# Optimization experiments

Hardware: AMD Instinct MI355X
Metric: run time of the kernel (lower is better)

## Reference

```python
import jax, jax.numpy as jnp
import numpy as np

B, D, H, W = 16, 512, 32, 32
M = 2000
TEMP_UPDATE = 0.1
TEMP_GATHER = 0.1


def l2norm(x, axis, eps=1e-12):
    # matches F.normalize: x / max(||x||_2, eps)
    n = jnp.linalg.norm(x, axis=axis, keepdims=True)
    return x / jnp.maximum(n, eps)


def setup_inputs() -> dict:
    key = jax.random.key(0)
    k1, k2 = jax.random.split(key)
    query = jax.random.normal(k1, (B, D, H, W), dtype=jnp.float32)
    # memory bank initialized as F.normalize(randn) * 0.1, as in __init__
    keys = l2norm(jax.random.normal(k2, (M, D), dtype=jnp.float32), axis=1) * 0.1
    return {"query": query, "keys": keys}


def reference(query, keys):
    b, d, h, w = query.shape
    m = keys.shape[0]
    # normalize along channels, move to [B,H,W,D], flatten to [N,D]
    q = jnp.transpose(l2norm(query, axis=1), (0, 2, 3, 1))
    qf = q.reshape(b * h * w, d)  # [N, D]

    # --- get_score (same score reused by gather_loss / read / update) ---
    score = l2norm(qf, axis=1) @ l2norm(keys, axis=1).T  # [N, M] cosine sims
    tg = min(max(TEMP_GATHER, 1e-8), 1.0)
    tu = min(max(TEMP_UPDATE, 1e-8), 1.0)
    score_query = jax.nn.softmax(score / tg, axis=0)   # softmax over queries
    score_memory = jax.nn.softmax(score / tu, axis=1)  # softmax over memory slots

    # --- gather_loss (train) ---
    _, top2 = jax.lax.top_k(score_memory, 2)  # [N, 2]
    pos = jax.lax.stop_gradient(keys[top2[:, 0]])
    neg = jax.lax.stop_gradient(keys[top2[:, 1]])
    compactness_loss = jnp.mean((qf - pos) ** 2)
    # TripletMarginLoss(margin=1.0), torch pairwise_distance eps=1e-6
    dp = jnp.sqrt(jnp.sum((qf - pos + 1e-6) ** 2, axis=-1))
    dn = jnp.sqrt(jnp.sum((qf - neg + 1e-6) ** 2, axis=-1))
    separateness_loss = jnp.mean(jnp.maximum(dp - dn + 1.0, 0.0))

    # --- read ---
    concat_memory = jax.lax.stop_gradient(score_memory) @ keys  # [N, D]
    updated_query = jnp.concatenate([qf, concat_memory], axis=1)
    updated_query = jnp.transpose(updated_query.reshape(b, h, w, 2 * d), (0, 3, 1, 2))

    # --- update (vectorized get_update_query: per-slot gather + weighted sum) ---
    g = top2[:, 0]  # top-1 gathering index per query, [N]
    col_max = jnp.max(score_query, axis=0)  # [M]
    w_raw = jnp.take_along_axis(score_query, g[:, None], axis=1)[:, 0] / (col_max[g] + 1e-8)
    denom = jax.ops.segment_sum(w_raw, g, num_segments=m) + 1e-8  # [M]
    weights = w_raw / denom[g]
    query_update = jax.ops.segment_sum(weights[:, None] * qf, g, num_segments=m)  # [M, D]
    updated_memory = jax.lax.stop_gradient(l2norm(query_update + keys, axis=1))

    return (updated_query, updated_memory, score_query, score_memory,
            separateness_loss, compactness_loss)
```

## Files before the change

### kernel.cpp

```cpp
#include <hip/hip_runtime.h>
#include <math.h>

#define NQ 16384
#define DD 512
#define MM 2000
#define MPAD 2048
#define KPAD 2048

#define UQ_OFF   0
#define UM_OFF   16777216
#define SQ_OFF   17801216
#define SM_OFF   50569216
#define SEP_OFF  83337216
#define COMP_OFF 83337217

typedef unsigned short u16;
typedef __attribute__((ext_vector_type(8))) short bhalf8;
typedef __attribute__((ext_vector_type(4))) float f32x4;

__device__ float    g_qf[NQ * DD];
__device__ float    g_keyshat[MM * DD];
__device__ int      g_top1[NQ];
__device__ int      g_top2[NQ];
__device__ unsigned g_colmax[MM];
__device__ float    g_colsum[MM];
__device__ float    g_rowsum[NQ];
__device__ float    g_wraw[NQ];
__device__ float    g_denom[MM];
__device__ float    g_bins[128];
__device__ int      g_cnt[MM];
__device__ int      g_cursor[MM];
__device__ int      g_base[MM];
__device__ int      g_rows[NQ];
__device__ float    g_wvals[NQ];

__device__ __attribute__((aligned(16))) u16 g_qh[NQ * DD];
__device__ __attribute__((aligned(16))) u16 g_ql[NQ * DD];
__device__ __attribute__((aligned(16))) u16 g_kh[MPAD * DD];
__device__ __attribute__((aligned(16))) u16 g_kl[MPAD * DD];
__device__ __attribute__((aligned(16))) u16 g_kth[DD * KPAD];
__device__ __attribute__((aligned(16))) u16 g_ktl[DD * KPAD];
__device__ __attribute__((aligned(16))) u16 g_smh[(size_t)NQ * KPAD];
__device__ __attribute__((aligned(16))) u16 g_sml[(size_t)NQ * KPAD];

__device__ inline u16 f32_to_bf16(float x) {
    unsigned u = __float_as_uint(x);
    return (u16)((u + 0x7fffu + ((u >> 16) & 1u)) >> 16);
}
__device__ inline float bf16f(u16 h) { return __uint_as_float((unsigned)h << 16); }

__device__ __forceinline__ void gl_lds16(const void* g, void* l) {
    __builtin_amdgcn_global_load_lds(
        (const __attribute__((address_space(1))) void*)g,
        (__attribute__((address_space(3))) void*)l, 16, 0, 0);
}

__global__ __launch_bounds__(256) void init_kernel() {
    int i = blockIdx.x * 256 + threadIdx.x;
    if (i < MM) { g_colsum[i] = 0.f; g_denom[i] = 0.f; g_colmax[i] = 0u;
                  g_cnt[i] = 0; g_cursor[i] = 0; }
    if (i < 128) g_bins[i] = 0.f;
    if (i < NQ) g_rowsum[i] = 0.f;
}

__global__ __launch_bounds__(256) void keys_norm_kernel(const float* __restrict__ keys) {
    int m = blockIdx.x, t = threadIdx.x;
    float v0 = keys[m * DD + t], v1 = keys[m * DD + t + 256];
    __shared__ float red[256];
    red[t] = v0 * v0 + v1 * v1;
    __syncthreads();
    for (int s = 128; s > 0; s >>= 1) { if (t < s) red[t] += red[t + s]; __syncthreads(); }
    float inv = 1.f / fmaxf(sqrtf(red[0]), 1e-12f);
    float n0 = v0 * inv, n1 = v1 * inv;
    g_keyshat[m * DD + t]       = n0;
    g_keyshat[m * DD + t + 256] = n1;
    u16 h0 = f32_to_bf16(n0), h1 = f32_to_bf16(n1);
    g_kh[(size_t)m * DD + t]       = h0;
    g_kl[(size_t)m * DD + t]       = f32_to_bf16(n0 - bf16f(h0));
    g_kh[(size_t)m * DD + t + 256] = h1;
    g_kl[(size_t)m * DD + t + 256] = f32_to_bf16(n1 - bf16f(h1));
}

__global__ __launch_bounds__(256) void ktrans_kernel(const float* __restrict__ keys) {
    __shared__ float tile[32][33];
    int tx = threadIdx.x & 31, ty = threadIdx.x >> 5;
    int c0 = blockIdx.x * 32;
    int m0 = blockIdx.y * 32;
    for (int i = ty; i < 32; i += 8) {
        int m = m0 + i;
        tile[i][tx] = (m < MM) ? keys[(size_t)m * DD + c0 + tx] : 0.f;
    }
    __syncthreads();
    for (int i = ty; i < 32; i += 8) {
        int c = c0 + i;
        float v = tile[tx][i];
        u16 h = f32_to_bf16(v);
        g_kth[(size_t)c * KPAD + m0 + tx] = h;
        g_ktl[(size_t)c * KPAD + m0 + tx] = f32_to_bf16(v - bf16f(h));
    }
}

__global__ __launch_bounds__(256) void qnorm_kernel(const float* __restrict__ q, float* __restrict__ out) {
    int bh = blockIdx.x; int b = bh >> 5, h = bh & 31;
    int t = threadIdx.x; int w = t & 31, dl = t >> 5;
    const float* qb = q + (size_t)b * DD * 1024 + h * 32;

    float ss = 0.f;
    for (int d = dl; d < DD; d += 8) { float v = qb[d * 1024 + w]; ss = fmaf(v, v, ss); }
    __shared__ float red[8][32];
    __shared__ float sinv[32];
    red[dl][w] = ss;
    __syncthreads();
    if (dl == 0) {
        float tot = 0.f;
        #pragma unroll
        for (int j = 0; j < 8; ++j) tot += red[j][w];
        sinv[w] = 1.f / fmaxf(sqrtf(tot), 1e-12f);
    }
    __syncthreads();

    __shared__ float tile[32][33];
    int dcol = t & 31, wl = t >> 5;
    for (int d0 = 0; d0 < DD; d0 += 32) {
        for (int dd = dl; dd < 32; dd += 8) {
            float v = qb[(d0 + dd) * 1024 + w] * sinv[w];
            tile[dd][w] = v;
            out[UQ_OFF + (size_t)((b << 10) + d0 + dd) * 1024 + (h << 5) + w] = v;
        }
        __syncthreads();
        for (int wr = wl; wr < 32; wr += 8) {
            float v = tile[dcol][wr];
            size_t idx = ((size_t)b * 1024 + h * 32 + wr) * DD + d0 + dcol;
            g_qf[idx] = v;
            u16 hh = f32_to_bf16(v);
            g_qh[idx] = hh;
            g_ql[idx] = f32_to_bf16(v - bf16f(hh));
        }
        __syncthreads();
    }
}

__device__ inline void mfma_block(const u16 (*Ah)[64], const u16 (*Al)[64],
                                  const u16 (*Bh)[64], const u16 (*Bl)[64],
                                  int wr, int wc, int l15, int hi, f32x4 acc[4][4]) {
    for (int sub = 0; sub < 2; ++sub) {
        bhalf8 a_h[4], a_l[4], b_h[4], b_l[4];
        #pragma unroll
        for (int i = 0; i < 4; ++i) {
            int r = wr + i * 16 + l15;
            int ps = (((sub << 2) | hi) ^ (r & 7)) << 3;
            a_h[i] = *(const bhalf8*)&Ah[r][ps];
            a_l[i] = *(const bhalf8*)&Al[r][ps];
        }
        #pragma unroll
        for (int j = 0; j < 4; ++j) {
            int c = wc + j * 16 + l15;
            int ps = (((sub << 2) | hi) ^ (c & 7)) << 3;
            b_h[j] = *(const bhalf8*)&Bh[c][ps];
            b_l[j] = *(const bhalf8*)&Bl[c][ps];
        }
        #pragma unroll
        for (int i = 0; i < 4; ++i)
            #pragma unroll
            for (int j = 0; j < 4; ++j) {
                acc[i][j] = __builtin_amdgcn_mfma_f32_16x16x32_bf16(a_h[i], b_h[j], acc[i][j], 0, 0, 0);
                acc[i][j] = __builtin_amdgcn_mfma_f32_16x16x32_bf16(a_h[i], b_l[j], acc[i][j], 0, 0, 0);
                acc[i][j] = __builtin_amdgcn_mfma_f32_16x16x32_bf16(a_l[i], b_h[j], acc[i][j], 0, 0, 0);
            }
    }
}

__global__ __launch_bounds__(256, 2) void gemm1_mfma(float* __restrict__ out) {
    __shared__ __attribute__((aligned(16))) u16 Ah[128][64];
    __shared__ __attribute__((aligned(16))) u16 Al[128][64];
    __shared__ __attribute__((aligned(16))) u16 Bh[128][64];
    __shared__ __attribute__((aligned(16))) u16 Bl[128][64];
    int t = threadIdx.x;
    int lane = t & 63, wv = t >> 6;
    int wr = (wv >> 1) << 6, wc = (wv & 1) << 6;
    int l15 = lane & 15, hi = lane >> 4;
    int row0 = blockIdx.x * 128;
    int col0 = blockIdx.y * 128;

    f32x4 acc[4][4] = {};
    int lr = lane >> 3, sslot = lane & 7;
    int xs = sslot ^ lr;

    for (int k0 = 0; k0 < DD; k0 += 64) {
        #pragma unroll
        for (int p = 0; p < 4; ++p) {
            int r = wv * 8 + lr + p * 32;
            size_t ga = (size_t)(row0 + r) * DD + k0 + xs * 8;
            size_t gb = (size_t)(col0 + r) * DD + k0 + xs * 8;
            gl_lds16(g_qh + ga, &Ah[p * 32 + wv * 8][0]);
            gl_lds16(g_ql + ga, &Al[p * 32 + wv * 8][0]);
            gl_lds16(g_kh + gb, &Bh[p * 32 + wv * 8][0]);
            gl_lds16(g_kl + gb, &Bl[p * 32 + wv * 8][0]);
        }
        __syncthreads();
        mfma_block(Ah, Al, Bh, Bl, wr, wc, l15, hi, acc);
        __syncthreads();
    }

    float rowp[4][4];
    #pragma unroll
    for (int i = 0; i < 4; ++i)
        #pragma unroll
        for (int q = 0; q < 4; ++q) rowp[i][q] = 0.f;

    #pragma unroll
    for (int j = 0; j < 4; ++j) {
        int c = col0 + wc + j * 16 + l15;
        bool valid = (c < MM);
        float cs = 0.f, cm = 0.f;
        #pragma unroll
        for (int i = 0; i < 4; ++i) {
            int rbase = row0 + wr + i * 16 + hi * 4;
            #pragma unroll
            for (int q = 0; q < 4; ++q) {
                float e = __expf((acc[i][j][q] - 1.0f) * 10.0f);
                if (valid) out[SQ_OFF + (size_t)(rbase + q) * MM + c] = e;
                float ev = valid ? e : 0.f;
                rowp[i][q] += ev;
                cs += ev;
                cm = fmaxf(cm, ev);
            }
        }
        cs += __shfl_xor(cs, 16); cs += __shfl_xor(cs, 32);
        cm = fmaxf(cm, __shfl_xor(cm, 16)); cm = fmaxf(cm, __shfl_xor(cm, 32));
        if (hi == 0 && valid) {
            atomicAdd(&g_colsum[c], cs);
            atomicMax(&g_colmax[c], __float_as_uint(cm));
        }
    }
    #pragma unroll
    for (int i = 0; i < 4; ++i)
        #pragma unroll
        for (int q = 0; q < 4; ++q) {
            float v = rowp[i][q];
            v += __shfl_xor(v, 1); v += __shfl_xor(v, 2);
            v += __shfl_xor(v, 4); v += __shfl_xor(v, 8);
            if (l15 == 0) atomicAdd(&g_rowsum[row0 + wr + i * 16 + hi * 4 + q], v);
        }
}

__global__ __launch_bounds__(256) void rowpass_kernel(float* __restrict__ out) {
    int n = blockIdx.x, t = threadIdx.x;
    __shared__ float rv[256], rv2[256];
    __shared__ int   ri[256], ri2[256];
    float inv_rs = 1.f / g_rowsum[n];
    float* raw = out + SQ_OFF + (size_t)n * MM;
    float* sm  = out + SM_OFF + (size_t)n * MM;
    float v1 = -1.f, v2 = -1.f; int i1 = 0x7fffffff, i2 = 0x7fffffff;
    #pragma unroll
    for (int i = 0; i < 8; ++i) {
        int idx = i * 256 + t;
        if (idx < MM) {
            float e = raw[idx];
            if (e > v1)      { v2 = v1; i2 = i1; v1 = e; i1 = idx; }
            else if (e > v2) { v2 = e; i2 = idx; }
            float smv = e * inv_rs;
            sm[idx] = smv;
            u16 hh = f32_to_bf16(smv);
            g_smh[(size_t)n * KPAD + idx] = hh;
            g_sml[(size_t)n * KPAD + idx] = f32_to_bf16(smv - bf16f(hh));
            raw[idx] = e / g_colsum[idx];
        }
    }
    rv[t] = v1; ri[t] = i1; rv2[t] = v2; ri2[t] = i2;
    __syncthreads();
    for (int s = 128; s > 0; s >>= 1) {
        if (t < s) {
            float av1 = rv[t],  bv1 = rv[t + s];
            float av2 = rv2[t], bv2 = rv2[t + s];
            int   ai1 = ri[t],  bi1 = ri[t + s];
            int   ai2 = ri2[t], bi2 = ri2[t + s];
            bool afirst = (av1 > bv1) || (av1 == bv1 && ai1 < bi1);
            float nv1, nv2; int ni1, ni2;
            if (afirst) {
                nv1 = av1; ni1 = ai1;
                if ((av2 > bv1) || (av2 == bv1 && ai2 < bi1)) { nv2 = av2; ni2 = ai2; }
                else                                          { nv2 = bv1; ni2 = bi1; }
            } else {
                nv1 = bv1; ni1 = bi1;
                if ((bv2 > av1) || (bv2 == av1 && bi2 < ai1)) { nv2 = bv2; ni2 = bi2; }
                else                                          { nv2 = av1; ni2 = ai1; }
            }
            rv[t] = nv1; ri[t] = ni1; rv2[t] = nv2; ri2[t] = ni2;
        }
        __syncthreads();
    }
    if (t == 0) { g_top1[n] = ri[0]; g_top2[n] = ri2[0]; }
}

__global__ __launch_bounds__(256) void rerank_loss_kernel(const float* __restrict__ keys) {
    int n = blockIdx.x * 4 + (threadIdx.x >> 6);
    int lane = threadIdx.x & 63;
    int i1 = g_top1[n], i2 = g_top2[n];
    const float* q  = g_qf      + (size_t)n  * DD;
    const float* k1 = g_keyshat + (size_t)i1 * DD;
    const float* k2 = g_keyshat + (size_t)i2 * DD;
    float s1 = 0.f, s2 = 0.f;
    #pragma unroll
    for (int kk = 0; kk < 8; ++kk) {
        int k = lane + kk * 64;
        float qv = q[k];
        s1 = fmaf(qv, k1[k], s1);
        s2 = fmaf(qv, k2[k], s2);
    }
    #pragma unroll
    for (int off = 1; off < 64; off <<= 1) {
        s1 += __shfl_xor(s1, off);
        s2 += __shfl_xor(s2, off);
    }
    bool sw = (s2 > s1) || (s2 == s1 && i2 < i1);
    int gi = sw ? i2 : i1, ni = sw ? i1 : i2;
    if (lane == 0 && sw) { g_top1[n] = i2; g_top2[n] = i1; }
    const float* kp = keys + (size_t)gi * DD;
    const float* kn = keys + (size_t)ni * DD;
    float comp = 0.f, dpp = 0.f, dnn = 0.f;
    #pragma unroll
    for (int kk = 0; kk < 8; ++kk) {
        int k = lane + kk * 64;
        float qv = q[k];
        float dq = qv - kp[k];
        comp = fmaf(dq, dq, comp);
        float a = dq + 1e-6f;
        dpp = fmaf(a, a, dpp);
        float b2 = qv - kn[k] + 1e-6f;
        dnn = fmaf(b2, b2, dnn);
    }
    #pragma unroll
    for (int off = 1; off < 64; off <<= 1) {
        comp += __shfl_xor(comp, off);
        dpp  += __shfl_xor(dpp,  off);
        dnn  += __shfl_xor(dnn,  off);
    }
    if (lane == 0) {
        float dp = sqrtf(dpp), dn = sqrtf(dnn);
        atomicAdd(&g_bins[n & 63], fmaxf(dp - dn + 1.0f, 0.0f));
        atomicAdd(&g_bins[64 + (n & 63)], comp);
    }
}

__global__ __launch_bounds__(256) void wraw_kernel(const float* __restrict__ out) {
    int n = blockIdx.x * 256 + threadIdx.x;
    int gi = g_top1[n];
    float sqv = out[SQ_OFF + (size_t)n * MM + gi];
    float cm = __uint_as_float(g_colmax[gi]) / g_colsum[gi];
    float w = sqv / (cm + 1e-8f);
    g_wraw[n] = w;
    atomicAdd(&g_denom[gi], w);
    atomicAdd(&g_cnt[gi], 1);
}

__global__ __launch_bounds__(256) void scan_kernel() {
    int t = threadIdx.x;
    __shared__ int chunk[256];
    __shared__ int off[256];
    int loc[8];
    int s = 0;
    #pragma unroll
    for (int i = 0; i < 8; ++i) {
        int idx = t * 8 + i;
        int c = (idx < MM) ? g_cnt[idx] : 0;
        loc[i] = s; s += c;
    }
    chunk[t] = s;
    __syncthreads();
    if (t == 0) {
        int acc = 0;
        for (int i = 0; i < 256; ++i) { off[i] = acc; acc += chunk[i]; }
    }
    __syncthreads();
    #pragma unroll
    for (int i = 0; i < 8; ++i) {
        int idx = t * 8 + i;
        if (idx < MM) g_base[idx] = off[t] + loc[i];
    }
}

__global__ __launch_bounds__(256) void scatter_kernel() {
    int n = blockIdx.x * 256 + threadIdx.x;
    int gi = g_top1[n];
    int pos = atomicAdd(&g_cursor[gi], 1);
    int dst = g_base[gi] + pos;
    g_rows[dst]  = n;
    g_wvals[dst] = g_wraw[n];
}

__global__ __launch_bounds__(256) void seg_update_kernel(const float* __restrict__ keys, float* __restrict__ out) {
    int m = blockIdx.x, t = threadIdx.x;
    int start = g_base[m], cnt = g_cnt[m];
    float invd = 1.f / (g_denom[m] + 1e-8f);
    float acc0 = 0.f, acc1 = 0.f;
    for (int i = 0; i < cnt; ++i) {
        int   row = g_rows[start + i];
        float wgt = g_wvals[start + i] * invd;
        acc0 = fmaf(wgt, g_qf[(size_t)row * DD + t],       acc0);
        acc1 = fmaf(wgt, g_qf[(size_t)row * DD + t + 256], acc1);
    }
    float v0 = acc0 + keys[m * DD + t];
    float v1 = acc1 + keys[m * DD + t + 256];
    __shared__ float red[256];
    red[t] = v0 * v0 + v1 * v1;
    __syncthreads();
    for (int s = 128; s > 0; s >>= 1) { if (t < s) red[t] += red[t + s]; __syncthreads(); }
    float inv = 1.f / fmaxf(sqrtf(red[0]), 1e-12f);
    out[UM_OFF + (size_t)m * DD + t]       = v0 * inv;
    out[UM_OFF + (size_t)m * DD + t + 256] = v1 * inv;
}

__global__ __launch_bounds__(256, 2) void gemm2_mfma(float* __restrict__ out) {
    __shared__ __attribute__((aligned(16))) u16 Ah[128][64];
    __shared__ __attribute__((aligned(16))) u16 Al[128][64];
    __shared__ __attribute__((aligned(16))) u16 Bh[128][64];
    __shared__ __attribute__((aligned(16))) u16 Bl[128][64];
    int t = threadIdx.x;
    int lane = t & 63, wv = t >> 6;
    int wr = (wv >> 1) << 6, wc = (wv & 1) << 6;
    int l15 = lane & 15, hi = lane >> 4;
    int row0 = blockIdx.x * 128;
    int col0 = blockIdx.y * 128;

    f32x4 acc[4][4] = {};
    int lr = lane >> 3, sslot = lane & 7;
    int xs = sslot ^ lr;

    for (int k0 = 0; k0 < KPAD; k0 += 64) {
        #pragma unroll
        for (int p = 0; p < 4; ++p) {
            int r = wv * 8 + lr + p * 32;
            size_t ga = (size_t)(row0 + r) * KPAD + k0 + xs * 8;
            size_t gb = (size_t)(col0 + r) * KPAD + k0 + xs * 8;
            gl_lds16(g_kth + ga, &Ah[p * 32 + wv * 8][0]);
            gl_lds16(g_ktl + ga, &Al[p * 32 + wv * 8][0]);
            gl_lds16(g_smh + gb, &Bh[p * 32 + wv * 8][0]);
            gl_lds16(g_sml + gb, &Bl[p * 32 + wv * 8][0]);
        }
        __syncthreads();
        mfma_block(Ah, Al, Bh, Bl, wr, wc, l15, hi, acc);
        __syncthreads();
    }
    int bq = col0 >> 10;
    #pragma unroll
    for (int i = 0; i < 4; ++i) {
        int chb = row0 + wr + i * 16 + hi * 4;
        #pragma unroll
        for (int j = 0; j < 4; ++j) {
            int n = col0 + wc + j * 16 + l15;
            size_t base = UQ_OFF + ((size_t)(bq * 1024 + 512 + chb)) * 1024 + (n & 1023);
            #pragma unroll
            for (int q = 0; q < 4; ++q)
                out[base + (size_t)q * 1024] = acc[i][j][q];
        }
    }
}

__global__ __launch_bounds__(64) void finalize_kernel(float* __restrict__ out) {
    if (threadIdx.x == 0) {
        float s = 0.f, c = 0.f;
        for (int i = 0; i < 64; ++i) { s += g_bins[i]; c += g_bins[64 + i]; }
        out[SEP_OFF]  = s / (float)NQ;
        out[COMP_OFF] = c / ((float)NQ * (float)DD);
    }
}

extern "C" void kernel_launch(void* const* d_in, const int* in_sizes, int n_in,
                              void* d_out, int out_size, void* d_ws, size_t ws_size,
                              hipStream_t stream) {
    const float* query = (const float*)d_in[0];
    const float* keys  = (const float*)d_in[1];
    float* out = (float*)d_out;

    init_kernel<<<dim3(64), dim3(256), 0, stream>>>();
    keys_norm_kernel<<<dim3(MM), dim3(256), 0, stream>>>(keys);
    ktrans_kernel<<<dim3(16, 63), dim3(256), 0, stream>>>(keys);
    qnorm_kernel<<<dim3(512), dim3(256), 0, stream>>>(query, out);
    gemm1_mfma<<<dim3(128, 16), dim3(256), 0, stream>>>(out);
    rowpass_kernel<<<dim3(NQ), dim3(256), 0, stream>>>(out);
    rerank_loss_kernel<<<dim3(NQ / 4), dim3(256), 0, stream>>>(keys);
    wraw_kernel<<<dim3(64), dim3(256), 0, stream>>>(out);
    scan_kernel<<<dim3(1), dim3(256), 0, stream>>>();
    scatter_kernel<<<dim3(64), dim3(256), 0, stream>>>();
    seg_update_kernel<<<dim3(MM), dim3(256), 0, stream>>>(keys, out);
    gemm2_mfma<<<dim3(4, 128), dim3(256), 0, stream>>>(out);
    finalize_kernel<<<dim3(1), dim3(64), 0, stream>>>(out);
}
```

Before: 971.9 us.

## Store unnormalized exp scores as split bf16, defer row normalization, double-buffer GEMMs

gemm1 now writes the exponentiated scores as hi/lo bf16 pairs into the GEMM2 operand buffers instead of fp32 to the output. The row pass reads these back with vector loads to produce both softmax outputs. gemm2 consumes the unnormalized scores and applies the per-row inverse sum in its epilogue. Both GEMMs switch to a K=32 double-buffered LDS pipeline that overlaps the next stage's loads with MFMA, and qnorm handles 64 pixels per block; together these cut fp32 round-trips and expose memory latency less, at the cost of a slight bf16-split rounding on score values.

```diff
diff --git a/kernel.cpp b/kernel.cpp
--- a/kernel.cpp
+++ b/kernel.cpp
@@ -25,6 +25,7 @@
 __device__ unsigned g_colmax[MM];
 __device__ float    g_colsum[MM];
 __device__ float    g_rowsum[NQ];
+__device__ float    g_invrs[NQ];
 __device__ float    g_wraw[NQ];
 __device__ float    g_denom[MM];
 __device__ float    g_bins[128];
@@ -101,36 +102,41 @@
 }
 
 __global__ __launch_bounds__(256) void qnorm_kernel(const float* __restrict__ q, float* __restrict__ out) {
-    int bh = blockIdx.x; int b = bh >> 5, h = bh & 31;
-    int t = threadIdx.x; int w = t & 31, dl = t >> 5;
-    const float* qb = q + (size_t)b * DD * 1024 + h * 32;
+    int blk = blockIdx.x;
+    int b = blk >> 4, hp = blk & 15;
+    int r0 = hp * 64;
+    int t = threadIdx.x;
+    int px = t & 63, ds = t >> 6;
+    const float* qb = q + (size_t)b * DD * 1024 + r0;
 
     float ss = 0.f;
-    for (int d = dl; d < DD; d += 8) { float v = qb[d * 1024 + w]; ss = fmaf(v, v, ss); }
-    __shared__ float red[8][32];
-    __shared__ float sinv[32];
-    red[dl][w] = ss;
-    __syncthreads();
-    if (dl == 0) {
-        float tot = 0.f;
-        #pragma unroll
-        for (int j = 0; j < 8; ++j) tot += red[j][w];
-        sinv[w] = 1.f / fmaxf(sqrtf(tot), 1e-12f);
-    }
-    __syncthreads();
-
-    __shared__ float tile[32][33];
-    int dcol = t & 31, wl = t >> 5;
+    for (int d = ds; d < DD; d += 4) { float v = qb[(size_t)d * 1024 + px]; ss = fmaf(v, v, ss); }
+    __shared__ float red[4][64];
+    __shared__ float sinv[64];
+    red[ds][px] = ss;
+    __syncthreads();
+    if (ds == 0) {
+        float tot = red[0][px] + red[1][px] + red[2][px] + red[3][px];
+        sinv[px] = 1.f / fmaxf(sqrtf(tot), 1e-12f);
+    }
+    __syncthreads();
+
+    __shared__ float tile[32][65];
+    int dcol = t & 31, pl = t >> 5;
     for (int d0 = 0; d0 < DD; d0 += 32) {
-        for (int dd = dl; dd < 32; dd += 8) {
-            float v = qb[(d0 + dd) * 1024 + w] * sinv[w];
-            tile[dd][w] = v;
-            out[UQ_OFF + (size_t)((b << 10) + d0 + dd) * 1024 + (h << 5) + w] = v;
+        #pragma unroll
+        for (int k = 0; k < 8; ++k) {
+            int dd = ds * 8 + k;
+            float v = qb[(size_t)(d0 + dd) * 1024 + px] * sinv[px];
+            tile[dd][px] = v;
+            out[UQ_OFF + (size_t)((b << 10) + d0 + dd) * 1024 + r0 + px] = v;
         }
         __syncthreads();
-        for (int wr = wl; wr < 32; wr += 8) {
-            float v = tile[dcol][wr];
-            size_t idx = ((size_t)b * 1024 + h * 32 + wr) * DD + d0 + dcol;
+        #pragma unroll
+        for (int pr = 0; pr < 8; ++pr) {
+            int px2 = pr * 8 + pl;
+            float v = tile[dcol][px2];
+            size_t idx = ((size_t)b * 1024 + r0 + px2) * DD + d0 + dcol;
             g_qf[idx] = v;
             u16 hh = f32_to_bf16(v);
             g_qh[idx] = hh;
@@ -140,65 +146,72 @@
     }
 }
 
-__device__ inline void mfma_block(const u16 (*Ah)[64], const u16 (*Al)[64],
-                                  const u16 (*Bh)[64], const u16 (*Bl)[64],
-                                  int wr, int wc, int l15, int hi, f32x4 acc[4][4]) {
-    for (int sub = 0; sub < 2; ++sub) {
-        bhalf8 a_h[4], a_l[4], b_h[4], b_l[4];
-        #pragma unroll
-        for (int i = 0; i < 4; ++i) {
-            int r = wr + i * 16 + l15;
-            int ps = (((sub << 2) | hi) ^ (r & 7)) << 3;
-            a_h[i] = *(const bhalf8*)&Ah[r][ps];
-            a_l[i] = *(const bhalf8*)&Al[r][ps];
-        }
+__device__ __forceinline__ void stage_pair(const u16* __restrict__ gh, const u16* __restrict__ gl,
+                                           u16 (*th)[32], u16 (*tl)[32],
+                                           size_t grow0, size_t ld, int kk, int wv, int lane) {
+    #pragma unroll
+    for (int p = 0; p < 2; ++p) {
+        int rbase = wv * 32 + p * 16;
+        int row = rbase + (lane >> 2);
+        int slot = (lane & 3) ^ ((row >> 1) & 3);
+        size_t off = (grow0 + row) * ld + (size_t)kk * 32 + slot * 8;
+        gl_lds16(gh + off, &th[rbase][0]);
+        gl_lds16(gl + off, &tl[rbase][0]);
+    }
+}
+
+__device__ __forceinline__ bhalf8 frag(const u16 (*tile)[32], int r, int hi) {
+    int ps = (hi ^ ((r >> 1) & 3)) << 3;
+    return *(const bhalf8*)&tile[r][ps];
+}
+
+__device__ __forceinline__ void mfma_phase(const u16 (*Ah)[32], const u16 (*Al)[32],
+                                           const u16 (*Bh)[32], const u16 (*Bl)[32],
+                                           int wr, int wc, int l15, int hi, f32x4 acc[4][4]) {
+    bhalf8 a_h[4], a_l[4], b_h[4], b_l[4];
+    #pragma unroll
+    for (int i = 0; i < 4; ++i) {
+        int r = wr + i * 16 + l15;
+        a_h[i] = frag(Ah, r, hi); a_l[i] = frag(Al, r, hi);
+    }
+    #pragma unroll
+    for (int j = 0; j < 4; ++j) {
+        int c = wc + j * 16 + l15;
+        b_h[j] = frag(Bh, c, hi); b_l[j] = frag(Bl, c, hi);
+    }
+    #pragma unroll
+    for (int i = 0; i < 4; ++i)
         #pragma unroll
         for (int j = 0; j < 4; ++j) {
-            int c = wc + j * 16 + l15;
-            int ps = (((sub << 2) | hi) ^ (c & 7)) << 3;
-            b_h[j] = *(const bhalf8*)&Bh[c][ps];
-            b_l[j] = *(const bhalf8*)&Bl[c][ps];
-        }
-        #pragma unroll
-        for (int i = 0; i < 4; ++i)
-            #pragma unroll
-            for (int j = 0; j < 4; ++j) {
-                acc[i][j] = __builtin_amdgcn_mfma_f32_16x16x32_bf16(a_h[i], b_h[j], acc[i][j], 0, 0, 0);
-                acc[i][j] = __builtin_amdgcn_mfma_f32_16x16x32_bf16(a_h[i], b_l[j], acc[i][j], 0, 0, 0);
-                acc[i][j] = __builtin_amdgcn_mfma_f32_16x16x32_bf16(a_l[i], b_h[j], acc[i][j], 0, 0, 0);
-            }
-    }
-}
-
-__global__ __launch_bounds__(256, 2) void gemm1_mfma(float* __restrict__ out) {
-    __shared__ __attribute__((aligned(16))) u16 Ah[128][64];
-    __shared__ __attribute__((aligned(16))) u16 Al[128][64];
-    __shared__ __attribute__((aligned(16))) u16 Bh[128][64];
-    __shared__ __attribute__((aligned(16))) u16 Bl[128][64];
-    int t = threadIdx.x;
-    int lane = t & 63, wv = t >> 6;
+            acc[i][j] = __builtin_amdgcn_mfma_f32_16x16x32_bf16(a_h[i], b_h[j], acc[i][j], 0, 0, 0);
+            acc[i][j] = __builtin_amdgcn_mfma_f32_16x16x32_bf16(a_h[i], b_l[j], acc[i][j], 0, 0, 0);
+            acc[i][j] = __builtin_amdgcn_mfma_f32_16x16x32_bf16(a_l[i], b_h[j], acc[i][j], 0, 0, 0);
+        }
+}
+
+__global__ __launch_bounds__(256, 2) void gemm1_mfma() {
+    __shared__ __attribute__((aligned(16))) u16 Ah[2][128][32];
+    __shared__ __attribute__((aligned(16))) u16 Al[2][128][32];
+    __shared__ __attribute__((aligned(16))) u16 Bh[2][128][32];
+    __shared__ __attribute__((aligned(16))) u16 Bl[2][128][32];
+    int t = threadIdx.x, lane = t & 63, wv = t >> 6;
     int wr = (wv >> 1) << 6, wc = (wv & 1) << 6;
     int l15 = lane & 15, hi = lane >> 4;
     int row0 = blockIdx.x * 128;
     int col0 = blockIdx.y * 128;
 
     f32x4 acc[4][4] = {};
-    int lr = lane >> 3, sslot = lane & 7;
-    int xs = sslot ^ lr;
-
-    for (int k0 = 0; k0 < DD; k0 += 64) {
-        #pragma unroll
-        for (int p = 0; p < 4; ++p) {
-            int r = wv * 8 + lr + p * 32;
-            size_t ga = (size_t)(row0 + r) * DD + k0 + xs * 8;
-            size_t gb = (size_t)(col0 + r) * DD + k0 + xs * 8;
-            gl_lds16(g_qh + ga, &Ah[p * 32 + wv * 8][0]);
-            gl_lds16(g_ql + ga, &Al[p * 32 + wv * 8][0]);
-            gl_lds16(g_kh + gb, &Bh[p * 32 + wv * 8][0]);
-            gl_lds16(g_kl + gb, &Bl[p * 32 + wv * 8][0]);
-        }
-        __syncthreads();
-        mfma_block(Ah, Al, Bh, Bl, wr, wc, l15, hi, acc);
+    stage_pair(g_qh, g_ql, Ah[0], Al[0], row0, DD, 0, wv, lane);
+    stage_pair(g_kh, g_kl, Bh[0], Bl[0], col0, DD, 0, wv, lane);
+    __syncthreads();
+    #pragma unroll 2
+    for (int kk = 0; kk < 16; ++kk) {
+        int cb = kk & 1, nb = cb ^ 1;
+        if (kk < 15) {
+            stage_pair(g_qh, g_ql, Ah[nb], Al[nb], row0, DD, kk + 1, wv, lane);
+            stage_pair(g_kh, g_kl, Bh[nb], Bl[nb], col0, DD, kk + 1, wv, lane);
+        }
+        mfma_phase(Ah[cb], Al[cb], Bh[cb], Bl[cb], wr, wc, l15, hi, acc);
         __syncthreads();
     }
 
@@ -219,8 +232,14 @@
             #pragma unroll
             for (int q = 0; q < 4; ++q) {
                 float e = __expf((acc[i][j][q] - 1.0f) * 10.0f);
-                if (valid) out[SQ_OFF + (size_t)(rbase + q) * MM + c] = e;
-                float ev = valid ? e : 0.f;
+                u16 eh = f32_to_bf16(e);
+                u16 el = f32_to_bf16(e - bf16f(eh));
+                float er = bf16f(eh) + bf16f(el);
+                if (valid) {
+                    g_smh[(size_t)(rbase + q) * KPAD + c] = eh;
+                    g_sml[(size_t)(rbase + q) * KPAD + c] = el;
+                }
+                float ev = valid ? er : 0.f;
                 rowp[i][q] += ev;
                 cs += ev;
                 cm = fmaxf(cm, ev);
@@ -246,25 +265,36 @@
 
 __global__ __launch_bounds__(256) void rowpass_kernel(float* __restrict__ out) {
     int n = blockIdx.x, t = threadIdx.x;
+    float inv_rs = 1.f / g_rowsum[n];
+    if (t == 0) g_invrs[n] = inv_rs;
     __shared__ float rv[256], rv2[256];
     __shared__ int   ri[256], ri2[256];
-    float inv_rs = 1.f / g_rowsum[n];
-    float* raw = out + SQ_OFF + (size_t)n * MM;
-    float* sm  = out + SM_OFF + (size_t)n * MM;
-    float v1 = -1.f, v2 = -1.f; int i1 = 0x7fffffff, i2 = 0x7fffffff;
-    #pragma unroll
-    for (int i = 0; i < 8; ++i) {
-        int idx = i * 256 + t;
-        if (idx < MM) {
-            float e = raw[idx];
-            if (e > v1)      { v2 = v1; i2 = i1; v1 = e; i1 = idx; }
-            else if (e > v2) { v2 = e; i2 = idx; }
-            float smv = e * inv_rs;
-            sm[idx] = smv;
-            u16 hh = f32_to_bf16(smv);
-            g_smh[(size_t)n * KPAD + idx] = hh;
-            g_sml[(size_t)n * KPAD + idx] = f32_to_bf16(smv - bf16f(hh));
-            raw[idx] = e / g_colsum[idx];
+    float v1 = -1.f, v2 = -2.f; int i1 = 0x7fffffff, i2 = 0x7fffffff;
+    int i8 = t * 8;
+    if (i8 < MM) {
+        uint4 hv = *(const uint4*)&g_smh[(size_t)n * KPAD + i8];
+        uint4 lv = *(const uint4*)&g_sml[(size_t)n * KPAD + i8];
+        unsigned hw[4] = {hv.x, hv.y, hv.z, hv.w};
+        unsigned lw[4] = {lv.x, lv.y, lv.z, lv.w};
+        float e[8];
+        #pragma unroll
+        for (int k = 0; k < 4; ++k) {
+            e[2 * k]     = __uint_as_float(hw[k] << 16)         + __uint_as_float(lw[k] << 16);
+            e[2 * k + 1] = __uint_as_float(hw[k] & 0xffff0000u) + __uint_as_float(lw[k] & 0xffff0000u);
+        }
+        #pragma unroll
+        for (int k = 0; k < 8; ++k) {
+            float ek = e[k]; int idx = i8 + k;
+            if (ek > v1)      { v2 = v1; i2 = i1; v1 = ek; i1 = idx; }
+            else if (ek > v2) { v2 = ek; i2 = idx; }
+        }
+        float* smp = out + SM_OFF + (size_t)n * MM + i8;
+        float* sqp = out + SQ_OFF + (size_t)n * MM + i8;
+        const float* cs = g_colsum + i8;
+        #pragma unroll
+        for (int k = 0; k < 8; ++k) {
+            smp[k] = e[k] * inv_rs;
+            sqp[k] = e[k] / cs[k];
         }
     }
     rv[t] = v1; ri[t] = i1; rv2[t] = v2; ri2[t] = i2;
@@ -412,37 +442,34 @@
 }
 
 __global__ __launch_bounds__(256, 2) void gemm2_mfma(float* __restrict__ out) {
-    __shared__ __attribute__((aligned(16))) u16 Ah[128][64];
-    __shared__ __attribute__((aligned(16))) u16 Al[128][64];
-    __shared__ __attribute__((aligned(16))) u16 Bh[128][64];
-    __shared__ __attribute__((aligned(16))) u16 Bl[128][64];
-    int t = threadIdx.x;
-    int lane = t & 63, wv = t >> 6;
+    __shared__ __attribute__((aligned(16))) u16 Ah[2][128][32];
+    __shared__ __attribute__((aligned(16))) u16 Al[2][128][32];
+    __shared__ __attribute__((aligned(16))) u16 Bh[2][128][32];
+    __shared__ __attribute__((aligned(16))) u16 Bl[2][128][32];
+    int t = threadIdx.x, lane = t & 63, wv = t >> 6;
     int wr = (wv >> 1) << 6, wc = (wv & 1) << 6;
     int l15 = lane & 15, hi = lane >> 4;
     int row0 = blockIdx.x * 128;
     int col0 = blockIdx.y * 128;
 
     f32x4 acc[4][4] = {};
-    int lr = lane >> 3, sslot = lane & 7;
-    int xs = sslot ^ lr;
-
-    for (int k0 = 0; k0 < KPAD; k0 += 64) {
-        #pragma unroll
-        for (int p = 0; p < 4; ++p) {
-            int r = wv * 8 + lr + p * 32;
-            size_t ga = (size_t)(row0 + r) * KPAD + k0 + xs * 8;
-            size_t gb = (size_t)(col0 + r) * KPAD + k0 + xs * 8;
-            gl_lds16(g_kth + ga, &Ah[p * 32 + wv * 8][0]);
-            gl_lds16(g_ktl + ga, &Al[p * 32 + wv * 8][0]);
-            gl_lds16(g_smh + gb, &Bh[p * 32 + wv * 8][0]);
-            gl_lds16(g_sml + gb, &Bl[p * 32 + wv * 8][0]);
-        }
+    stage_pair(g_kth, g_ktl, Ah[0], Al[0], row0, KPAD, 0, wv, lane);
+    stage_pair(g_smh, g_sml, Bh[0], Bl[0], col0, KPAD, 0, wv, lane);
+    __syncthreads();
+    #pragma unroll 2
+    for (int kk = 0; kk < 64; ++kk) {
+        int cb = kk & 1, nb = cb ^ 1;
+        if (kk < 63) {
+            stage_pair(g_kth, g_ktl, Ah[nb], Al[nb], row0, KPAD, kk + 1, wv, lane);
+            stage_pair(g_smh, g_sml, Bh[nb], Bl[nb], col0, KPAD, kk + 1, wv, lane);
+        }
+        mfma_phase(Ah[cb], Al[cb], Bh[cb], Bl[cb], wr, wc, l15, hi, acc);
         __syncthreads();
-        mfma_block(Ah, Al, Bh, Bl, wr, wc, l15, hi, acc);
-        __syncthreads();
     }
     int bq = col0 >> 10;
+    float irs[4];
+    #pragma unroll
+    for (int j = 0; j < 4; ++j) irs[j] = g_invrs[col0 + wc + j * 16 + l15];
     #pragma unroll
     for (int i = 0; i < 4; ++i) {
         int chb = row0 + wr + i * 16 + hi * 4;
@@ -452,7 +479,7 @@
             size_t base = UQ_OFF + ((size_t)(bq * 1024 + 512 + chb)) * 1024 + (n & 1023);
             #pragma unroll
             for (int q = 0; q < 4; ++q)
-                out[base + (size_t)q * 1024] = acc[i][j][q];
+                out[base + (size_t)q * 1024] = acc[i][j][q] * irs[j];
         }
     }
 }
@@ -476,8 +503,8 @@
     init_kernel<<<dim3(64), dim3(256), 0, stream>>>();
     keys_norm_kernel<<<dim3(MM), dim3(256), 0, stream>>>(keys);
     ktrans_kernel<<<dim3(16, 63), dim3(256), 0, stream>>>(keys);
-    qnorm_kernel<<<dim3(512), dim3(256), 0, stream>>>(query, out);
-    gemm1_mfma<<<dim3(128, 16), dim3(256), 0, stream>>>(out);
+    qnorm_kernel<<<dim3(256), dim3(256), 0, stream>>>(query, out);
+    gemm1_mfma<<<dim3(128, 16), dim3(256), 0, stream>>>();
     rowpass_kernel<<<dim3(NQ), dim3(256), 0, stream>>>(out);
     rerank_loss_kernel<<<dim3(NQ / 4), dim3(256), 0, stream>>>(keys);
     wraw_kernel<<<dim3(64), dim3(256), 0, stream>>>(out);
```

Result: slower. 998.9 us (+2.8%).
